# Kernel optimization log

Measured on AMD Instinct MI355X. Metric: run time of the kernel, lower is better.

The kernel has to match this reference:

```python
import jax, jax.numpy as jnp
import numpy as np

L_MAX = 6
R = 1
IN_IRREPS  = [(256,0),(128,1),(128,2),(64,3),(64,4),(64,5),(64,6)]
HID_IRREPS = [(64,0),(64,1),(64,2),(32,3),(32,4),(32,5),(32,6)]
N_SCALARS = 64
N_GATES = sum(m for m, l in HID_IRREPS if l > 0)  # 256
PRE_IRREPS = [(N_SCALARS,0),(N_GATES,0)] + [(m,l) for m,l in HID_IRREPS if l > 0]
OUT_IRREPS = [(R,l) for l in range(L_MAX+1)]

def _dim(irr):
    return sum(m*(2*l+1) for m, l in irr)

def _wsize(in_irr, out_irr):
    mul_in = {l: m for m, l in in_irr}
    return sum(mul_in[l]*mo for mo, l in out_irr)

def e3linear(x, wflat, in_irr, out_irr):
    # block-diagonal per-irrep linear with e3nn 1/sqrt(fan_in) normalization
    B = x.shape[0]
    blocks = {}
    off = 0
    for mul, l in in_irr:
        d = mul*(2*l+1)
        blocks[l] = (x[:, off:off+d].reshape(B, mul, 2*l+1), mul)
        off += d
    outs = []
    woff = 0
    for mul_out, l in out_irr:
        xb, mul_in = blocks[l]
        w = wflat[woff:woff+mul_in*mul_out].reshape(mul_in, mul_out)
        woff += mul_in*mul_out
        y = jnp.einsum('bim,io->bom', xb, w) * (1.0/np.sqrt(mul_in))
        outs.append(y.reshape(B, mul_out*(2*l+1)))
    return jnp.concatenate(outs, axis=1)

def gate(z):
    # z = [scalars 64x0e | gates 256x0e | gated l>0 irreps]
    s = jax.nn.silu(z[:, :N_SCALARS])
    g = jax.nn.sigmoid(z[:, N_SCALARS:N_SCALARS+N_GATES])
    x = z[:, N_SCALARS+N_GATES:]
    outs = [s]
    goff = 0
    xoff = 0
    for mul, l in HID_IRREPS:
        if l == 0:
            continue
        m = 2*l+1
        xb = x[:, xoff:xoff+mul*m].reshape(-1, mul, m)
        outs.append((xb * g[:, goff:goff+mul, None]).reshape(-1, mul*m))
        goff += mul
        xoff += mul*m
    return jnp.concatenate(outs, axis=1)

def _forward(v_raw, w1, w2, w3, w4):
    x = gate(e3linear(v_raw, w1, IN_IRREPS, PRE_IRREPS))
    x = gate(e3linear(x, w2, HID_IRREPS, PRE_IRREPS))
    x = gate(e3linear(x, w3, HID_IRREPS, PRE_IRREPS))
    c = e3linear(x, w4, HID_IRREPS, OUT_IRREPS)  # [B, 49]
    B = c.shape[0]
    segs = []
    off = 0
    for l in range(L_MAX+1):
        m = 2*l+1
        seg = c[:, off:off+R*m].reshape(B, R, m).transpose(0, 2, 1)  # (B, m, R)
        segs.append(seg)
        off += R*m
    return jnp.concatenate(segs, axis=1)  # (B, 49, R)

def setup_inputs():
    key = jax.random.key(0)
    ks = jax.random.split(key, 5)
    B = 16384
    return {
        "v_raw": jax.random.normal(ks[0], (B, _dim(IN_IRREPS)), jnp.float32),
        "w1": jax.random.normal(ks[1], (_wsize(IN_IRREPS, PRE_IRREPS),), jnp.float32),
        "w2": jax.random.normal(ks[2], (_wsize(HID_IRREPS, PRE_IRREPS),), jnp.float32),
        "w3": jax.random.normal(ks[3], (_wsize(HID_IRREPS, PRE_IRREPS),), jnp.float32),
        "w4": jax.random.normal(ks[4], (_wsize(HID_IRREPS, OUT_IRREPS),), jnp.float32),
    }

def reference(v_raw, w1, w2, w3, w4):
    return _forward(v_raw, w1, w2, w3, w4)
```

## Files before the change

kernel.cpp:

```cpp
#include <hip/hip_runtime.h>
#include <cstddef>


typedef _Float16 half8 __attribute__((ext_vector_type(8)));
typedef _Float16 half4 __attribute__((ext_vector_type(4)));
typedef float    f32x4 __attribute__((ext_vector_type(4)));
typedef float    fvec4 __attribute__((ext_vector_type(4)));

#define B_ROWS   16
#define IN_DIM   3840
#define OUT_COLS 49
#define GP  264
#define HSP 72

#define OFF_G1  0
#define OFF_G2  4224
#define OFF_G3  8448
#define OFF_HS1 12672
#define OFF_HS2 13824
#define SMEM_ELTS 14976

#define P2BASE 106496
#define P3BASE 139264

__global__ __launch_bounds__(256) void prep_weights(
    const float* __restrict__ w1, const float* __restrict__ w2,
    const float* __restrict__ w3, _Float16* __restrict__ packed)
{
  static const int K_[24]    = {256,256,128,128,64,64,64,64,  64,64,64,64,32,32,32,32,
                                64,64,64,64,32,32,32,32};
  static const int N_[24]    = {64,256,64,64,32,32,32,32,  64,256,64,64,32,32,32,32,
                                64,256,64,64,32,32,32,32};
  static const int woff_[24] = {0,16384,81920,90112,98304,100352,102400,104448,
                                0,4096,20480,24576,28672,29696,30720,31744,
                                0,4096,20480,24576,28672,29696,30720,31744};
  static const int poff_[24] = {0,16384,81920,90112,98304,100352,102400,104448,
                                106496,110592,126976,131072,135168,136192,137216,138240,
                                139264,143360,159744,163840,167936,168960,169984,171008};
  const int g = blockIdx.x * 256 + threadIdx.x;
  int bi = 0;
#pragma unroll
  for (int i = 1; i < 24; ++i) if (g * 8 >= poff_[i]) bi = i;
  const float* w = (bi < 8) ? w1 : ((bi < 16) ? w2 : w3);
  const int rel8 = g - poff_[bi] / 8;
  const int K = K_[bi], N = N_[bi];
  const float scale = 1.0f / sqrtf((float)K);
  half8 vv;
  if (bi < 8) {
    const int lane = rel8 & 63;
    const int fi   = rel8 >> 6;
    const int KF = K >> 5;
    const int kf = fi % KF;
    const int mt = fi / KF;
    const int k0 = kf * 32 + (lane >> 4) * 8;
    const int o  = mt * 16 + (lane & 15);
#pragma unroll
    for (int j = 0; j < 8; ++j)
      vv[j] = (_Float16)(w[woff_[bi] + (size_t)(k0 + j) * N + o] * scale);
  } else {
    const int f  = rel8 >> 5;
    const int lp = (rel8 & 31) << 1;
    const int KF16 = K >> 4;
    const int ks = f % KF16;
    const int mt = f / KF16;
#pragma unroll
    for (int t = 0; t < 2; ++t) {
      const int l  = lp + t;
      const int i0 = ks * 16 + (l >> 4) * 4;
      const int o  = mt * 16 + (l & 15);
#pragma unroll
      for (int j = 0; j < 4; ++j)
        vv[t * 4 + j] = (_Float16)(w[woff_[bi] + (size_t)(i0 + j) * N + o] * scale);
    }
  }
  *(half8*)(packed + (size_t)g * 8) = vv;
}

template<int L> struct CP {
  static constexpr int TWOL1 = 2 * L + 1;
  static constexpr int K1  = (L <= 2) ? 128 : 64;
  static constexpr int N1  = (L <= 2) ? 64  : 32;
  static constexpr int KF1 = K1 / 32;
  static constexpr int MT  = N1 / 16;
  static constexpr int INOFF = (L==1)?256:(L==2)?640:(L==3)?1280:(L==4)?1728:(L==5)?2304:3008;
  static constexpr int P1    = (L==1)?81920:(L==2)?90112:(L==3)?98304:(L==4)?100352:(L==5)?102400:104448;
  static constexpr int P2R   = (L==1)?20480:(L==2)?24576:(L==3)?28672:(L==4)?29696:(L==5)?30720:31744;
  static constexpr int GO    = (L==1)?0:(L==2)?64:(L==3)?128:(L==4)?160:(L==5)?192:224;
  static constexpr int W4O   = (L==1)?64:(L==2)?128:(L==3)?192:(L==4)?224:(L==5)?256:288;
  static constexpr float SCALE = (N1 == 64) ? 0.125f : 0.17677669529663687f;
};

template<int L>
__device__ __forceinline__ void unit_load(const float* __restrict__ vraw,
                                          int b0, int ct, float (&rg)[CP<L>::KF1 * 8])
{
  using P = CP<L>;
  const int lane = threadIdx.x & 63;
  const int col  = lane & 15;
  const int quad = lane >> 4;
  const int c = ct * 16 + col;
  const int b = c / P::TWOL1;
  const int m = c - b * P::TWOL1;
  const float* base = vraw + (size_t)(b0 + b) * IN_DIM + P::INOFF + m
                    + (size_t)(quad * 8) * P::TWOL1;
#pragma unroll
  for (int kf = 0; kf < P::KF1; ++kf)
#pragma unroll
    for (int j = 0; j < 8; ++j)
      rg[kf * 8 + j] = base[(size_t)(kf * 32 + j) * P::TWOL1];
}

template<int L>
__device__ __forceinline__ void unit_compute(
    const float (&rg)[CP<L>::KF1 * 8], const _Float16* __restrict__ pk,
    const _Float16* G1, const _Float16* G2, const _Float16* G3,
    const float* __restrict__ w4, float* __restrict__ out, int b0, int ct)
{
  using P = CP<L>;
  const int lane = threadIdx.x & 63;
  const int col  = lane & 15;
  const int quad = lane >> 4;
  const int c = ct * 16 + col;
  const int b = c / P::TWOL1;
  const int m = c - b * P::TWOL1;
  half8 bf[P::KF1];
#pragma unroll
  for (int kf = 0; kf < P::KF1; ++kf)
#pragma unroll
    for (int j = 0; j < 8; ++j) bf[kf][j] = (_Float16)rg[kf * 8 + j];

  half4 ph1[P::MT];
#pragma unroll
  for (int mt = 0; mt < P::MT; ++mt) {
    f32x4 acc = {0.f, 0.f, 0.f, 0.f};
#pragma unroll
    for (int kf = 0; kf < P::KF1; ++kf) {
      const half8 av = *(const half8*)(pk + P::P1 + (size_t)((mt * P::KF1 + kf) * 64 + lane) * 8);
      acc = __builtin_amdgcn_mfma_f32_16x16x32_f16(av, bf[kf], acc, 0, 0, 0);
    }
    const int o0 = mt * 16 + quad * 4;
    const half4 g4 = *(const half4*)(G1 + b * GP + P::GO + o0);
    half4 h;
#pragma unroll
    for (int r = 0; r < 4; ++r) h[r] = (_Float16)(acc[r] * (float)g4[r]);
    ph1[mt] = h;
  }

  half4 ph2[P::MT];
#pragma unroll
  for (int mt = 0; mt < P::MT; ++mt) {
    f32x4 acc = {0.f, 0.f, 0.f, 0.f};
#pragma unroll
    for (int ks = 0; ks < P::MT; ++ks) {
      const half4 av = *(const half4*)(pk + P2BASE + P::P2R + (size_t)((mt * P::MT + ks) * 64 + lane) * 4);
      acc = __builtin_amdgcn_mfma_f32_16x16x16f16(av, ph1[ks], acc, 0, 0, 0);
    }
    const int o0 = mt * 16 + quad * 4;
    const half4 g4 = *(const half4*)(G2 + b * GP + P::GO + o0);
    half4 h;
#pragma unroll
    for (int r = 0; r < 4; ++r) h[r] = (_Float16)(acc[r] * (float)g4[r]);
    ph2[mt] = h;
  }

  float s = 0.f;
#pragma unroll
  for (int mt = 0; mt < P::MT; ++mt) {
    f32x4 acc = {0.f, 0.f, 0.f, 0.f};
#pragma unroll
    for (int ks = 0; ks < P::MT; ++ks) {
      const half4 av = *(const half4*)(pk + P3BASE + P::P2R + (size_t)((mt * P::MT + ks) * 64 + lane) * 4);
      acc = __builtin_amdgcn_mfma_f32_16x16x16f16(av, ph2[ks], acc, 0, 0, 0);
    }
    const int o0 = mt * 16 + quad * 4;
    const half4 g4 = *(const half4*)(G3 + b * GP + P::GO + o0);
#pragma unroll
    for (int r = 0; r < 4; ++r)
      s += acc[r] * (float)g4[r] * w4[P::W4O + o0 + r];
  }
  s += __shfl_xor(s, 16, 64);
  s += __shfl_xor(s, 32, 64);
  if (quad == 0)
    out[(size_t)(b0 + b) * OUT_COLS + L * L + m] = s * P::SCALE;
}

template<int L, int CT0, int NCT>
__device__ __forceinline__ void run_chain(
    const float* __restrict__ vraw, const _Float16* __restrict__ pk,
    const _Float16* G1, const _Float16* G2, const _Float16* G3,
    const float* __restrict__ w4, float* __restrict__ out, int b0)
{
  float rg[2][CP<L>::KF1 * 8];
  unit_load<L>(vraw, b0, CT0, rg[0]);
#pragma unroll
  for (int u = 0; u < NCT; ++u) {
    if (u + 1 < NCT) unit_load<L>(vraw, b0, CT0 + u + 1, rg[(u + 1) & 1]);
    unit_compute<L>(rg[u & 1], pk, G1, G2, G3, w4, out, b0, CT0 + u);
  }
}

template<int L, int CT0, int NCT>
__device__ __forceinline__ void run_chain_pre(
    const float* __restrict__ vraw, const _Float16* __restrict__ pk,
    const _Float16* G1, const _Float16* G2, const _Float16* G3,
    const float* __restrict__ w4, float* __restrict__ out, int b0,
    const float (&pre)[CP<L>::KF1 * 8])
{
  float rg[2][CP<L>::KF1 * 8];
#pragma unroll
  for (int i = 0; i < CP<L>::KF1 * 8; ++i) rg[0][i] = pre[i];
#pragma unroll
  for (int u = 0; u < NCT; ++u) {
    if (u + 1 < NCT) unit_load<L>(vraw, b0, CT0 + u + 1, rg[(u + 1) & 1]);
    unit_compute<L>(rg[u & 1], pk, G1, G2, G3, w4, out, b0, CT0 + u);
  }
}

__device__ __forceinline__ void load_scal_frags(const float* __restrict__ vraw,
                                                int b0, half8 (&sf)[8])
{
  const int lane = threadIdx.x & 63;
  const int col  = lane & 15;
  const int quad = lane >> 4;
  const float* base = vraw + (size_t)(b0 + col) * IN_DIM + quad * 8;
#pragma unroll
  for (int kf = 0; kf < 8; ++kf) {
    const fvec4 a = *(const fvec4*)(base + kf * 32);
    const fvec4 b2 = *(const fvec4*)(base + kf * 32 + 4);
#pragma unroll
    for (int j = 0; j < 4; ++j) { sf[kf][j] = (_Float16)a[j]; sf[kf][4 + j] = (_Float16)b2[j]; }
  }
}

__device__ __forceinline__ void scal_L1(const half8 (&sf)[8],
    const _Float16* __restrict__ pk, _Float16* Hs1, _Float16* G1v)
{
  const int lane = threadIdx.x & 63;
  const int wv   = threadIdx.x >> 6;
  const int col  = lane & 15;
  const int quad = lane >> 4;
  {
    f32x4 acc = {0.f, 0.f, 0.f, 0.f};
#pragma unroll
    for (int kf = 0; kf < 8; ++kf) {
      const half8 av = *(const half8*)(pk + (size_t)((wv * 8 + kf) * 64 + lane) * 8);
      acc = __builtin_amdgcn_mfma_f32_16x16x32_f16(av, sf[kf], acc, 0, 0, 0);
    }
    const int o0 = wv * 16 + quad * 4;
    half4 h;
#pragma unroll
    for (int r = 0; r < 4; ++r) { const float z = acc[r]; h[r] = (_Float16)(z / (1.f + __expf(-z))); }
    *(half4*)(Hs1 + col * HSP + o0) = h;
  }
#pragma unroll
  for (int t = 0; t < 4; ++t) {
    const int mt = wv * 4 + t;
    f32x4 acc = {0.f, 0.f, 0.f, 0.f};
#pragma unroll
    for (int kf = 0; kf < 8; ++kf) {
      const half8 av = *(const half8*)(pk + 16384 + (size_t)((mt * 8 + kf) * 64 + lane) * 8);
      acc = __builtin_amdgcn_mfma_f32_16x16x32_f16(av, sf[kf], acc, 0, 0, 0);
    }
    const int o0 = mt * 16 + quad * 4;
    half4 g;
#pragma unroll
    for (int r = 0; r < 4; ++r) g[r] = (_Float16)(1.f / (1.f + __expf(-acc[r])));
    *(half4*)(G1v + col * GP + o0) = g;
  }
}

__device__ __forceinline__ void scal_mid(const _Float16* HsIn,
    const _Float16* __restrict__ pkS, const _Float16* __restrict__ pkG,
    _Float16* HsOut, _Float16* Gv)
{
  const int lane = threadIdx.x & 63;
  const int wv   = threadIdx.x >> 6;
  const int col  = lane & 15;
  const int quad = lane >> 4;
  half4 bf4[4];
#pragma unroll
  for (int ks = 0; ks < 4; ++ks)
    bf4[ks] = *(const half4*)(HsIn + col * HSP + ks * 16 + quad * 4);
  {
    f32x4 acc = {0.f, 0.f, 0.f, 0.f};
#pragma unroll
    for (int ks = 0; ks < 4; ++ks) {
      const half4 av = *(const half4*)(pkS + (size_t)((wv * 4 + ks) * 64 + lane) * 4);
      acc = __builtin_amdgcn_mfma_f32_16x16x16f16(av, bf4[ks], acc, 0, 0, 0);
    }
    const int o0 = wv * 16 + quad * 4;
    half4 h;
#pragma unroll
    for (int r = 0; r < 4; ++r) { const float z = acc[r]; h[r] = (_Float16)(z / (1.f + __expf(-z))); }
    *(half4*)(HsOut + col * HSP + o0) = h;
  }
#pragma unroll
  for (int t = 0; t < 4; ++t) {
    const int mt = wv * 4 + t;
    f32x4 acc = {0.f, 0.f, 0.f, 0.f};
#pragma unroll
    for (int ks = 0; ks < 4; ++ks) {
      const half4 av = *(const half4*)(pkG + (size_t)((mt * 4 + ks) * 64 + lane) * 4);
      acc = __builtin_amdgcn_mfma_f32_16x16x16f16(av, bf4[ks], acc, 0, 0, 0);
    }
    const int o0 = mt * 16 + quad * 4;
    half4 g;
#pragma unroll
    for (int r = 0; r < 4; ++r) g[r] = (_Float16)(1.f / (1.f + __expf(-acc[r])));
    *(half4*)(Gv + col * GP + o0) = g;
  }
}

__device__ __forceinline__ void scal_last(const _Float16* Hs2,
    const _Float16* __restrict__ pkS, const _Float16* __restrict__ pkG,
    _Float16* G3v, const float* __restrict__ w4, float* __restrict__ out, int b0)
{
  const int lane = threadIdx.x & 63;
  const int wv   = threadIdx.x >> 6;
  const int col  = lane & 15;
  const int quad = lane >> 4;
  half4 bf4[4];
#pragma unroll
  for (int ks = 0; ks < 4; ++ks)
    bf4[ks] = *(const half4*)(Hs2 + col * HSP + ks * 16 + quad * 4);
  if (wv == 0) {
    float s = 0.f;
#pragma unroll
    for (int mt = 0; mt < 4; ++mt) {
      f32x4 acc = {0.f, 0.f, 0.f, 0.f};
#pragma unroll
      for (int ks = 0; ks < 4; ++ks) {
        const half4 av = *(const half4*)(pkS + (size_t)((mt * 4 + ks) * 64 + lane) * 4);
        acc = __builtin_amdgcn_mfma_f32_16x16x16f16(av, bf4[ks], acc, 0, 0, 0);
      }
      const int o0 = mt * 16 + quad * 4;
#pragma unroll
      for (int r = 0; r < 4; ++r) {
        const float z = acc[r];
        s += (z / (1.f + __expf(-z))) * w4[o0 + r];
      }
    }
    s += __shfl_xor(s, 16, 64);
    s += __shfl_xor(s, 32, 64);
    if (quad == 0) out[(size_t)(b0 + col) * OUT_COLS] = s * 0.125f;
  } else {
    const int t0 = (wv == 1) ? 0 : (wv == 2) ? 6 : 11;
    const int tn = (wv == 1) ? 6 : 5;
    for (int t = 0; t < tn; ++t) {
      const int mt = t0 + t;
      f32x4 acc = {0.f, 0.f, 0.f, 0.f};
#pragma unroll
      for (int ks = 0; ks < 4; ++ks) {
        const half4 av = *(const half4*)(pkG + (size_t)((mt * 4 + ks) * 64 + lane) * 4);
        acc = __builtin_amdgcn_mfma_f32_16x16x16f16(av, bf4[ks], acc, 0, 0, 0);
      }
      const int o0 = mt * 16 + quad * 4;
      half4 g;
#pragma unroll
      for (int r = 0; r < 4; ++r) g[r] = (_Float16)(1.f / (1.f + __expf(-acc[r])));
      *(half4*)(G3v + col * GP + o0) = g;
    }
  }
}

__global__ __launch_bounds__(256, 2) void fused_decoder(
    const float* __restrict__ vraw, const float* __restrict__ w4,
    const _Float16* __restrict__ pk, float* __restrict__ out)
{
  __shared__ __align__(16) _Float16 smem[SMEM_ELTS];
  _Float16* G1  = smem + OFF_G1;
  _Float16* G2  = smem + OFF_G2;
  _Float16* G3  = smem + OFF_G3;
  _Float16* Hs1 = smem + OFF_HS1;
  _Float16* Hs2 = smem + OFF_HS2;
  const int wv = threadIdx.x >> 6;
  const int b0 = blockIdx.x * B_ROWS;

  half8 sf[8];
  load_scal_frags(vraw, b0, sf);

  float pre[32];
  if (wv == 0)      unit_load<2>(vraw, b0, 0, reinterpret_cast<float(&)[32]>(pre));
  else if (wv == 1) unit_load<1>(vraw, b0, 0, reinterpret_cast<float(&)[32]>(pre));
  else if (wv == 2) unit_load<6>(vraw, b0, 0, reinterpret_cast<float(&)[16]>(pre));
  else              unit_load<5>(vraw, b0, 0, reinterpret_cast<float(&)[16]>(pre));

  scal_L1(sf, pk, Hs1, G1);
  __syncthreads();
  scal_mid(Hs1, pk + P2BASE, pk + P2BASE + 4096, Hs2, G2);
  __syncthreads();
  scal_last(Hs2, pk + P3BASE, pk + P3BASE + 4096, G3, w4, out, b0);
  __syncthreads();

  if (wv == 0) {
    run_chain_pre<2, 0, 5>(vraw, pk, G1, G2, G3, w4, out, b0,
                           reinterpret_cast<float(&)[32]>(pre));
    run_chain<3, 0, 4>(vraw, pk, G1, G2, G3, w4, out, b0);
  } else if (wv == 1) {
    run_chain_pre<1, 0, 3>(vraw, pk, G1, G2, G3, w4, out, b0,
                           reinterpret_cast<float(&)[32]>(pre));
    run_chain<3, 4, 3>(vraw, pk, G1, G2, G3, w4, out, b0);
    run_chain<4, 0, 5>(vraw, pk, G1, G2, G3, w4, out, b0);
  } else if (wv == 2) {
    run_chain_pre<6, 0, 13>(vraw, pk, G1, G2, G3, w4, out, b0,
                            reinterpret_cast<float(&)[16]>(pre));
    run_chain<4, 5, 1>(vraw, pk, G1, G2, G3, w4, out, b0);
  } else {
    run_chain_pre<5, 0, 11>(vraw, pk, G1, G2, G3, w4, out, b0,
                            reinterpret_cast<float(&)[16]>(pre));
    run_chain<4, 6, 3>(vraw, pk, G1, G2, G3, w4, out, b0);
  }
}

extern "C" void kernel_launch(void* const* d_in, const int* in_sizes, int n_in,
                              void* d_out, int out_size, void* d_ws, size_t ws_size,
                              hipStream_t stream)
{
  (void)in_sizes; (void)n_in; (void)out_size; (void)ws_size;
  const float* vraw = (const float*)d_in[0];
  const float* w1   = (const float*)d_in[1];
  const float* w2   = (const float*)d_in[2];
  const float* w3   = (const float*)d_in[3];
  const float* w4   = (const float*)d_in[4];
  float* out = (float*)d_out;
  _Float16* packed = (_Float16*)d_ws;

  prep_weights<<<84, 256, 0, stream>>>(w1, w2, w3, packed);
  fused_decoder<<<16384 / B_ROWS, 256, 0, stream>>>(vraw, w4, packed, out);
}
```

Before: 388.2 us.

## Cut register pressure to allow four blocks per CU

The double-buffered fp32 prefetch registers are replaced by a single fp32 temp. Each tile is converted to fp16 fragments before the next tile's load is issued into that temp. The early prefetch of the first vector tile, which overlapped the scalar-path layers, is dropped, and launch bounds are raised from 2 to 4 blocks per SM. The aim is higher occupancy hiding global load latency instead of explicit prefetching. The risk is that it loses the load overlap with the scalar phase and may cause spills under the tighter register budget.

Result: slower. 412.4 us (+6.2%).

```diff
diff --git a/kernel.cpp b/kernel.cpp
--- a/kernel.cpp
+++ b/kernel.cpp
@@ -92,7 +92,7 @@
 
 template<int L>
 __device__ __forceinline__ void unit_load(const float* __restrict__ vraw,
-                                          int b0, int ct, float (&rg)[CP<L>::KF1 * 8])
+                                          int b0, int ct, float (&tmp)[CP<L>::KF1 * 8])
 {
   using P = CP<L>;
   const int lane = threadIdx.x & 63;
@@ -107,12 +107,22 @@
   for (int kf = 0; kf < P::KF1; ++kf)
 #pragma unroll
     for (int j = 0; j < 8; ++j)
-      rg[kf * 8 + j] = base[(size_t)(kf * 32 + j) * P::TWOL1];
+      tmp[kf * 8 + j] = base[(size_t)(kf * 32 + j) * P::TWOL1];
+}
+
+template<int L>
+__device__ __forceinline__ void cvt_frags(const float (&tmp)[CP<L>::KF1 * 8],
+                                          half8 (&bf)[CP<L>::KF1])
+{
+#pragma unroll
+  for (int kf = 0; kf < CP<L>::KF1; ++kf)
+#pragma unroll
+    for (int j = 0; j < 8; ++j) bf[kf][j] = (_Float16)tmp[kf * 8 + j];
 }
 
 template<int L>
 __device__ __forceinline__ void unit_compute(
-    const float (&rg)[CP<L>::KF1 * 8], const _Float16* __restrict__ pk,
+    const half8 (&bf)[CP<L>::KF1], const _Float16* __restrict__ pk,
     const _Float16* G1, const _Float16* G2, const _Float16* G3,
     const float* __restrict__ w4, float* __restrict__ out, int b0, int ct)
 {
@@ -123,11 +133,6 @@
   const int c = ct * 16 + col;
   const int b = c / P::TWOL1;
   const int m = c - b * P::TWOL1;
-  half8 bf[P::KF1];
-#pragma unroll
-  for (int kf = 0; kf < P::KF1; ++kf)
-#pragma unroll
-    for (int j = 0; j < 8; ++j) bf[kf][j] = (_Float16)rg[kf * 8 + j];
 
   half4 ph1[P::MT];
 #pragma unroll
@@ -190,29 +195,14 @@
     const _Float16* G1, const _Float16* G2, const _Float16* G3,
     const float* __restrict__ w4, float* __restrict__ out, int b0)
 {
-  float rg[2][CP<L>::KF1 * 8];
-  unit_load<L>(vraw, b0, CT0, rg[0]);
+  float tmp[CP<L>::KF1 * 8];
+  unit_load<L>(vraw, b0, CT0, tmp);
 #pragma unroll
   for (int u = 0; u < NCT; ++u) {
-    if (u + 1 < NCT) unit_load<L>(vraw, b0, CT0 + u + 1, rg[(u + 1) & 1]);
-    unit_compute<L>(rg[u & 1], pk, G1, G2, G3, w4, out, b0, CT0 + u);
-  }
-}
-
-template<int L, int CT0, int NCT>
-__device__ __forceinline__ void run_chain_pre(
-    const float* __restrict__ vraw, const _Float16* __restrict__ pk,
-    const _Float16* G1, const _Float16* G2, const _Float16* G3,
-    const float* __restrict__ w4, float* __restrict__ out, int b0,
-    const float (&pre)[CP<L>::KF1 * 8])
-{
-  float rg[2][CP<L>::KF1 * 8];
-#pragma unroll
-  for (int i = 0; i < CP<L>::KF1 * 8; ++i) rg[0][i] = pre[i];
-#pragma unroll
-  for (int u = 0; u < NCT; ++u) {
-    if (u + 1 < NCT) unit_load<L>(vraw, b0, CT0 + u + 1, rg[(u + 1) & 1]);
-    unit_compute<L>(rg[u & 1], pk, G1, G2, G3, w4, out, b0, CT0 + u);
+    half8 bf[CP<L>::KF1];
+    cvt_frags<L>(tmp, bf);
+    if (u + 1 < NCT) unit_load<L>(vraw, b0, CT0 + u + 1, tmp);
+    unit_compute<L>(bf, pk, G1, G2, G3, w4, out, b0, CT0 + u);
   }
 }
 
@@ -363,7 +353,7 @@
   }
 }
 
-__global__ __launch_bounds__(256, 2) void fused_decoder(
+__global__ __launch_bounds__(256, 4) void fused_decoder(
     const float* __restrict__ vraw, const float* __restrict__ w4,
     const _Float16* __restrict__ pk, float* __restrict__ out)
 {
@@ -378,13 +368,6 @@
 
   half8 sf[8];
   load_scal_frags(vraw, b0, sf);
-
-  float pre[32];
-  if (wv == 0)      unit_load<2>(vraw, b0, 0, reinterpret_cast<float(&)[32]>(pre));
-  else if (wv == 1) unit_load<1>(vraw, b0, 0, reinterpret_cast<float(&)[32]>(pre));
-  else if (wv == 2) unit_load<6>(vraw, b0, 0, reinterpret_cast<float(&)[16]>(pre));
-  else              unit_load<5>(vraw, b0, 0, reinterpret_cast<float(&)[16]>(pre));
-
   scal_L1(sf, pk, Hs1, G1);
   __syncthreads();
   scal_mid(Hs1, pk + P2BASE, pk + P2BASE + 4096, Hs2, G2);
@@ -393,21 +376,17 @@
   __syncthreads();
 
   if (wv == 0) {
-    run_chain_pre<2, 0, 5>(vraw, pk, G1, G2, G3, w4, out, b0,
-                           reinterpret_cast<float(&)[32]>(pre));
+    run_chain<2, 0, 5>(vraw, pk, G1, G2, G3, w4, out, b0);
     run_chain<3, 0, 4>(vraw, pk, G1, G2, G3, w4, out, b0);
   } else if (wv == 1) {
-    run_chain_pre<1, 0, 3>(vraw, pk, G1, G2, G3, w4, out, b0,
-                           reinterpret_cast<float(&)[32]>(pre));
+    run_chain<1, 0, 3>(vraw, pk, G1, G2, G3, w4, out, b0);
     run_chain<3, 4, 3>(vraw, pk, G1, G2, G3, w4, out, b0);
     run_chain<4, 0, 5>(vraw, pk, G1, G2, G3, w4, out, b0);
   } else if (wv == 2) {
-    run_chain_pre<6, 0, 13>(vraw, pk, G1, G2, G3, w4, out, b0,
-                            reinterpret_cast<float(&)[16]>(pre));
+    run_chain<6, 0, 13>(vraw, pk, G1, G2, G3, w4, out, b0);
     run_chain<4, 5, 1>(vraw, pk, G1, G2, G3, w4, out, b0);
   } else {
-    run_chain_pre<5, 0, 11>(vraw, pk, G1, G2, G3, w4, out, b0,
-                            reinterpret_cast<float(&)[16]>(pre));
+    run_chain<5, 0, 11>(vraw, pk, G1, G2, G3, w4, out, b0);
     run_chain<4, 6, 3>(vraw, pk, G1, G2, G3, w4, out, b0);
   }
 }
```
